# Optimization experiments

Hardware: AMD Instinct MI355X
Metric: run time of the kernel (lower is better)

## Reference

```python
import jax, jax.numpy as jnp
import numpy as np


def _att(xf, W1, W2):
    # xf: [B, L, dk]; low-rank attention scores, softmax over last dim
    dk = W1.shape[0]
    s1 = xf @ W1                                   # [B, L, 10]
    s2 = jnp.einsum('rk,bjk->brj', W2, xf)         # [B, 10, L]
    scores = jnp.einsum('bir,brj->bij', s1, s2) / jnp.sqrt(jnp.float32(dk))
    return jax.nn.softmax(scores, axis=-1)         # [B, L, L]


def setup_inputs() -> dict:
    B, Ci, Co, N, T = 8, 64, 64, 1000, 24
    ks = jax.random.split(jax.random.key(0), 16)
    f32 = jnp.float32
    return {
        'x': jax.random.normal(ks[0], (B, Ci, N, T), f32),
        'A_adj': jax.random.uniform(ks[1], (N, N), f32),
        'att0_W1': jax.random.normal(ks[2], (N * T, 10), f32) * 0.02,
        'att0_W2': jax.random.normal(ks[3], (10, N * T), f32) * 0.02,
        'gatt_W1': jax.random.normal(ks[4], (Ci * T, 10), f32) * 0.02,
        'gatt_W2': jax.random.normal(ks[5], (10, Ci * T), f32) * 0.02,
        'gcn_W': jax.random.normal(ks[6], (Ci, Co), f32) * 0.05,
        'tatt_W1': jax.random.normal(ks[7], (N * Co, 10), f32) * 0.02,
        'tatt_W2': jax.random.normal(ks[8], (10, N * Co), f32) * 0.02,
        'conv1_w': jax.random.normal(ks[9], (Co, Co, 1, 2), f32) * 0.05,
        'conv1_b': jax.random.normal(ks[10], (Co,), f32) * 0.05,
        'conv2_w': jax.random.normal(ks[11], (Co, Co, 1, 2), f32) * 0.05,
        'conv2_b': jax.random.normal(ks[12], (Co,), f32) * 0.05,
        'res_w': jax.random.normal(ks[13], (Co, Ci, 1, 1), f32) * 0.05,
        'res_b': jax.random.normal(ks[14], (Co,), f32) * 0.05,
        'ln_g': jnp.ones((Co,), f32),
        'ln_b': jnp.zeros((Co,), f32),
    }


def reference(x, A_adj, att0_W1, att0_W2, gatt_W1, gatt_W2, gcn_W,
              tatt_W1, tatt_W2, conv1_w, conv1_b, conv2_w, conv2_b,
              res_w, res_b, ln_g, ln_b):
    B, C, N, T = x.shape
    # ---- block-level channel attention (requires_value=True) ----
    xf = x.reshape(B, C, N * T)
    x1 = (_att(xf, att0_W1, att0_W2) @ xf).reshape(B, C, N, T)
    # ---- GCN block: attention-gated adjacency + graph matmul ----
    xg = jnp.transpose(x1, (0, 2, 1, 3)).reshape(B, N, C * T)
    Ag = _att(xg, gatt_W1, gatt_W2) * A_adj                  # [B, N, N]
    g1 = jnp.einsum('bnm,bcmt->bnct', Ag, x1)                # [B, N, C, T]
    g = jnp.einsum('bnct,co->bont', g1, gcn_W)               # [B, Co, N, T]
    Co = g.shape[1]
    # ---- TCN block: temporal attention + dilated causal convs ----
    xt = jnp.transpose(g, (0, 3, 2, 1)).reshape(B, T, N * Co)
    x2 = (_att(xt, tatt_W1, tatt_W2) @ xt).reshape(B, T, N, Co)
    x2 = jnp.transpose(x2, (0, 3, 2, 1))                     # [B, Co, N, T]
    for w, b, d in ((conv1_w, conv1_b, 1), (conv2_w, conv2_b, 2)):
        y = jax.lax.conv_general_dilated(
            x2, w, (1, 1), [(0, 0), (d, d)], rhs_dilation=(1, d),
            dimension_numbers=('NCHW', 'OIHW', 'NCHW'))
        y = y + b[None, :, None, None]
        x2 = jax.nn.relu(y[..., :-d])                        # trim to T
    # ---- 1x1 residual conv ----
    res = jnp.einsum('bcnt,oc->bont', x, res_w[:, :, 0, 0]) + res_b[None, :, None, None]
    out = jax.nn.relu(x2 + res)
    # ---- LayerNorm over channel dim ----
    o = jnp.transpose(out, (0, 3, 2, 1))                     # [B, T, N, Co]
    mu = o.mean(-1, keepdims=True)
    var = o.var(-1, keepdims=True)
    o = (o - mu) / jnp.sqrt(var + 1e-5) * ln_g + ln_b
    return jnp.transpose(o, (0, 3, 2, 1))                    # [B, Co, N, T]
```

## Files before the change

### kernel.cpp

```cpp
#include <hip/hip_runtime.h>
#include <hip/hip_bf16.h>

typedef unsigned int u32;
typedef unsigned short ushortt;

#define B_  8
#define C_  64
#define N_  1000
#define T_  24
#define R_  10
#define NT_ 24000
#define CT_ 1536
#define NC_ 64000

typedef __attribute__((ext_vector_type(8))) short bf8v;
typedef __attribute__((ext_vector_type(4))) float f4v;

__device__ __forceinline__ ushortt f2b_bits(float f) {
  u32 x = __float_as_uint(f);
  u32 r = (x + 0x7fffu + ((x >> 16) & 1u)) >> 16;
  return (ushortt)r;
}

__device__ __forceinline__ float blockSum256(float v, float* red) {
  red[threadIdx.x] = v; __syncthreads();
  #pragma unroll
  for (int s = 128; s > 0; s >>= 1) {
    if (threadIdx.x < s) red[threadIdx.x] += red[threadIdx.x + s];
    __syncthreads();
  }
  float r = red[0]; __syncthreads();
  return r;
}
__device__ __forceinline__ float blockMax256(float v, float* red) {
  red[threadIdx.x] = v; __syncthreads();
  #pragma unroll
  for (int s = 128; s > 0; s >>= 1) {
    if (threadIdx.x < s) red[threadIdx.x] = fmaxf(red[threadIdx.x], red[threadIdx.x + s]);
    __syncthreads();
  }
  float r = red[0]; __syncthreads();
  return r;
}

__device__ __forceinline__ void ld24f32(const float* p, float* v) {
  #pragma unroll
  for (int t = 0; t < 24; t += 4) {
    float4 f = *(const float4*)&p[t];
    v[t] = f.x; v[t+1] = f.y; v[t+2] = f.z; v[t+3] = f.w;
  }
}

__global__ __launch_bounds__(256) void zerok(float* p, int n) {
  int i = blockIdx.x * 256 + threadIdx.x;
  if (i < n) p[i] = 0.f;
}

__global__ __launch_bounds__(256) void pack_w(
    const float* __restrict__ W1, const float* __restrict__ W2,
    float* __restrict__ Wp, int K) {
  int i = blockIdx.x * 256 + threadIdx.x;
  if (i >= K * 20) return;
  int k = i / 20, r = i - k * 20;
  Wp[i] = (r < 10) ? W1[(size_t)k * 10 + r] : W2[(size_t)(r - 10) * K + k];
}

__global__ __launch_bounds__(256) void pack_tailw(
    const float* __restrict__ c1w, const float* __restrict__ c2w,
    const float* __restrict__ rw, ushortt* __restrict__ Wt) {
  int i = blockIdx.x * 256 + threadIdx.x;
  if (i >= 20480) return;
  float v;
  if (i < 8192) {
    int tap = i >> 12, o = (i >> 6) & 63, c = i & 63;
    v = c1w[(size_t)(o * 64 + c) * 2 + (tap ? 0 : 1)];
  } else if (i < 16384) {
    int j = i - 8192;
    int tap = j >> 12, o = (j >> 6) & 63, c = j & 63;
    v = c2w[(size_t)(o * 64 + c) * 2 + (tap ? 0 : 1)];
  } else {
    int j = i - 16384;
    v = rw[j];
  }
  Wt[i] = f2b_bits(v);
}

__global__ __launch_bounds__(256) void att0_s12(
    const float* __restrict__ x, const float* __restrict__ Wp,
    float* __restrict__ s1, float* __restrict__ s2) {
  __shared__ float red[40 * 257];
  const int row0 = blockIdx.x * 4;
  const int kbase = blockIdx.y * 6000;
  const int tid = threadIdx.x;
  float acc[4][20];
  #pragma unroll
  for (int r = 0; r < 4; ++r)
    #pragma unroll
    for (int j = 0; j < 20; ++j) acc[r][j] = 0.f;
  const float* xb = x + (size_t)row0 * NT_ + kbase;
  const float4* wb4 = (const float4*)Wp + (size_t)kbase * 5;
  #pragma unroll 1
  for (int it = 0; it < 6; ++it) {
    int slot = tid + 256 * it;
    if (slot < 1500) {
      int k = slot * 4;
      float4 xv0 = *(const float4*)&xb[k];
      float4 xv1 = *(const float4*)&xb[NT_ + k];
      float4 xv2 = *(const float4*)&xb[2 * NT_ + k];
      float4 xv3 = *(const float4*)&xb[3 * NT_ + k];
      const float4* w4 = wb4 + (size_t)slot * 20;
      #pragma unroll
      for (int kk = 0; kk < 4; ++kk) {
        float4 wa = w4[kk * 5 + 0], wbv = w4[kk * 5 + 1], wc = w4[kk * 5 + 2],
               wd = w4[kk * 5 + 3], we = w4[kk * 5 + 4];
        float w[20] = {wa.x,wa.y,wa.z,wa.w, wbv.x,wbv.y,wbv.z,wbv.w,
                       wc.x,wc.y,wc.z,wc.w, wd.x,wd.y,wd.z,wd.w,
                       we.x,we.y,we.z,we.w};
        float xs0 = ((const float*)&xv0)[kk];
        float xs1 = ((const float*)&xv1)[kk];
        float xs2 = ((const float*)&xv2)[kk];
        float xs3 = ((const float*)&xv3)[kk];
        #pragma unroll
        for (int j = 0; j < 20; ++j) {
          acc[0][j] += xs0 * w[j];
          acc[1][j] += xs1 * w[j];
          acc[2][j] += xs2 * w[j];
          acc[3][j] += xs3 * w[j];
        }
      }
    }
  }
  #pragma unroll
  for (int half = 0; half < 2; ++half) {
    __syncthreads();
    #pragma unroll
    for (int mm = 0; mm < 40; ++mm) {
      int m = half * 40 + mm;
      red[mm * 257 + tid] = acc[m / 20][m % 20];
    }
    __syncthreads();
    #pragma unroll
    for (int s = 128; s >= 8; s >>= 1) {
      for (int i = tid; i < 40 * s; i += 256) {
        int rr = i / s, col = i - rr * s;
        red[rr * 257 + col] += red[rr * 257 + col + s];
      }
      __syncthreads();
    }
    if (tid < 40) {
      float v = 0.f;
      #pragma unroll
      for (int c = 0; c < 8; ++c) v += red[tid * 257 + c];
      int m = half * 40 + tid;
      int row = row0 + m / 20, j = m % 20;
      if (j < 10) atomicAdd(&s1[row * 10 + j], v);
      else        atomicAdd(&s2[row * 10 + (j - 10)], v);
    }
  }
}

__global__ __launch_bounds__(64) void att0_softmax(
    const float* __restrict__ s1, const float* __restrict__ s2, float* __restrict__ P) {
  int b = blockIdx.x, i = threadIdx.x;
  float r1[R_];
  #pragma unroll
  for (int r = 0; r < R_; ++r) r1[r] = s1[(b * 64 + i) * R_ + r];
  const float scale = rsqrtf(24000.f);
  float row[64]; float m = -1e30f;
  for (int j = 0; j < 64; ++j) {
    const float* s2r = s2 + (size_t)(b * 64 + j) * R_;
    float d = 0.f;
    #pragma unroll
    for (int r = 0; r < R_; ++r) d += r1[r] * s2r[r];
    d *= scale; row[j] = d; m = fmaxf(m, d);
  }
  float s = 0.f;
  for (int j = 0; j < 64; ++j) { float e = __expf(row[j] - m); row[j] = e; s += e; }
  float inv = 1.f / s;
  for (int j = 0; j < 64; ++j) P[((size_t)b * 64 + i) * 64 + j] = row[j] * inv;
}

__global__ __launch_bounds__(256) void att0_apply(
    const float* __restrict__ x, const float* __restrict__ P, float* __restrict__ x1tr) {
  __shared__ float Pss[4160];
  __shared__ float xt[6144];
  int b = blockIdx.y, n0 = blockIdx.x * 4;
  int tid = threadIdx.x;
  for (int i = tid; i < 4096; i += 256)
    Pss[(i >> 6) * 65 + (i & 63)] = P[(size_t)b * 4096 + i];
  {
    const float4* src4 = (const float4*)x;
    float4* dst4 = (float4*)xt;
    for (int i = tid; i < 1536; i += 256) {
      int j = i / 24, q = i - j * 24;
      dst4[i] = src4[(size_t)(b * 64 + j) * 6000 + n0 * 6 + q];
    }
  }
  __syncthreads();
  int ig = tid >> 4, ln = (tid >> 2) & 3, ts = tid & 3;
  float acc[4][6];
  #pragma unroll
  for (int ii = 0; ii < 4; ++ii)
    #pragma unroll
    for (int m = 0; m < 6; ++m) acc[ii][m] = 0.f;
  const float* base = &xt[ln * 24 + ts * 6];
  #pragma unroll 4
  for (int j = 0; j < 64; ++j) {
    float vj[6];
    #pragma unroll
    for (int m = 0; m < 6; ++m) vj[m] = base[j * 96 + m];
    #pragma unroll
    for (int ii = 0; ii < 4; ++ii) {
      float p = Pss[(ig * 4 + ii) * 65 + j];
      #pragma unroll
      for (int m = 0; m < 6; ++m) acc[ii][m] += p * vj[m];
    }
  }
  float* drow = x1tr + ((size_t)b * N_ + n0 + ln) * CT_ + ts * 6;
  #pragma unroll
  for (int ii = 0; ii < 4; ++ii) {
    float* d = drow + (ig * 4 + ii) * 24;
    *(float2*)&d[0] = make_float2(acc[ii][0], acc[ii][1]);
    *(float2*)&d[2] = make_float2(acc[ii][2], acc[ii][3]);
    *(float2*)&d[4] = make_float2(acc[ii][4], acc[ii][5]);
  }
}

__global__ __launch_bounds__(256) void transpose_x1(
    const float* __restrict__ x1tr, ushortt* __restrict__ Xbt) {
  __shared__ float s[64][65];
  int b = blockIdx.z, n0 = blockIdx.y * 64, c0 = blockIdx.x * 64;
  int tid = threadIdx.x;
  int r = tid >> 2, cc = (tid & 3) * 16;
  if (n0 + r < N_) {
    const float* src = x1tr + ((size_t)b * N_ + n0 + r) * CT_ + c0 + cc;
    #pragma unroll
    for (int i = 0; i < 16; i += 4) {
      float4 v = *(const float4*)&src[i];
      s[r][cc + i] = v.x; s[r][cc + i + 1] = v.y;
      s[r][cc + i + 2] = v.z; s[r][cc + i + 3] = v.w;
    }
  } else {
    #pragma unroll
    for (int i = 0; i < 16; ++i) s[r][cc + i] = 0.f;
  }
  __syncthreads();
  ushortt* dst = Xbt + ((size_t)b * CT_ + c0 + r) * 1024 + n0 + cc;
  #pragma unroll
  for (int i = 0; i < 16; ++i) dst[i] = f2b_bits(s[cc + i][r]);
}

__global__ __launch_bounds__(256) void gatt_s12(
    const float* __restrict__ xg, const float* __restrict__ Wp,
    float* __restrict__ s1, float* __restrict__ s2T) {
  __shared__ float xs[6144];
  __shared__ float red[5120];
  int bn0 = blockIdx.x * 4;
  int tid = threadIdx.x;
  {
    const float4* src4 = (const float4*)(xg + (size_t)bn0 * CT_);
    float4* dst4 = (float4*)xs;
    for (int i = tid; i < 1536; i += 256) dst4[i] = src4[i];
  }
  __syncthreads();
  int rid = tid >> 6, ks = tid & 63;
  float a[20];
  #pragma unroll
  for (int r = 0; r < 20; ++r) a[r] = 0.f;
  for (int k = ks; k < CT_; k += 64) {
    float xv = xs[rid * CT_ + k];
    const float4* wp4 = (const float4*)&Wp[(size_t)k * 20];
    float4 wa = wp4[0], wb = wp4[1], wc = wp4[2], wd = wp4[3], we = wp4[4];
    float wv[20] = {wa.x,wa.y,wa.z,wa.w, wb.x,wb.y,wb.z,wb.w, wc.x,wc.y,wc.z,wc.w,
                    wd.x,wd.y,wd.z,wd.w, we.x,we.y,we.z,we.w};
    #pragma unroll
    for (int r = 0; r < 20; ++r) a[r] += xv * wv[r];
  }
  #pragma unroll
  for (int r = 0; r < 20; ++r) red[tid * 20 + r] = a[r];
  __syncthreads();
  if (tid < 80) {
    int rid2 = tid / 20, r = tid % 20;
    float s = 0.f;
    for (int l = 0; l < 64; ++l) s += red[(rid2 * 64 + l) * 20 + r];
    int row = bn0 + rid2;
    int b = row / N_, n = row - b * N_;
    if (r < 10) s1[row * 10 + r] = s;
    else        s2T[((size_t)b * 10 + (r - 10)) * N_ + n] = s;
  }
}

__global__ __launch_bounds__(256) void gatt_scores(
    const float* __restrict__ s1, const float* __restrict__ s2T,
    const float* __restrict__ Aadj, ushortt* __restrict__ Agb) {
  __shared__ float p[N_];
  __shared__ float r1[R_];
  __shared__ float red[256];
  int b = blockIdx.x / N_, n = blockIdx.x % N_;
  if (threadIdx.x < R_) r1[threadIdx.x] = s1[((size_t)b * N_ + n) * R_ + threadIdx.x];
  __syncthreads();
  const float scale = rsqrtf(1536.f);
  const float* s2b = s2T + (size_t)b * 10 * N_;
  float lmax = -1e30f;
  for (int m = threadIdx.x; m < N_; m += 256) {
    float d = 0.f;
    #pragma unroll
    for (int r = 0; r < R_; ++r) d += r1[r] * s2b[r * N_ + m];
    d *= scale; p[m] = d; lmax = fmaxf(lmax, d);
  }
  float gmax = blockMax256(lmax, red);
  float lsum = 0.f;
  for (int m = threadIdx.x; m < N_; m += 256) {
    float e = __expf(p[m] - gmax); p[m] = e; lsum += e;
  }
  float gsum = blockSum256(lsum, red);
  float inv = 1.f / gsum;
  ushortt* agr = Agb + ((size_t)b * 1024 + n) * 1024;
  const float* ar = Aadj + (size_t)n * N_;
  for (int m = threadIdx.x; m < 1024; m += 256) {
    float v = (m < N_) ? p[m] * inv * ar[m] : 0.f;
    agr[m] = f2b_bits(v);
  }
}

__global__ __launch_bounds__(256) void gemm_mfma(
    const ushortt* __restrict__ Agb, const ushortt* __restrict__ Xbt,
    float* __restrict__ g1) {
  __shared__ ushortt As[4096];
  __shared__ ushortt Bs[4096];
  const int b = blockIdx.z;
  const int n0 = blockIdx.x * 128;
  const int m0 = blockIdx.y * 128;
  const ushortt* Ab = Agb + (size_t)b * 1024 * 1024;
  const ushortt* Bb = Xbt + (size_t)b * 1536 * 1024;
  const int tid = threadIdx.x;
  const int wave = tid >> 6, lane = tid & 63;
  const int wr = (wave >> 1) * 64, wc = (wave & 1) * 64;
  const int lrow = lane >> 2;
  const int lcol = (lane & 3) * 8;
  const int q = lane >> 4, l15 = lane & 15;

  f4v acc[4][4];
  #pragma unroll
  for (int i = 0; i < 4; ++i)
    #pragma unroll
    for (int j = 0; j < 4; ++j) acc[i][j] = (f4v){0.f, 0.f, 0.f, 0.f};

  const ushortt* gA = Ab + (size_t)(m0 + wave * 16 + lrow) * 1024 + lcol;
  const ushortt* gB = Bb + (size_t)(n0 + wave * 16 + lrow) * 1024 + lcol;
  ushortt* lA = &As[wave * 16 * 32];
  ushortt* lB = &Bs[wave * 16 * 32];

  for (int k0 = 0; k0 < 1024; k0 += 32) {
    __syncthreads();
    __builtin_amdgcn_global_load_lds(
      (const __attribute__((address_space(1))) void*)(gA + k0),
      (__attribute__((address_space(3))) void*)lA, 16, 0, 0);
    __builtin_amdgcn_global_load_lds(
      (const __attribute__((address_space(1))) void*)(gA + (size_t)64 * 1024 + k0),
      (__attribute__((address_space(3))) void*)(lA + 64 * 32), 16, 0, 0);
    __builtin_amdgcn_global_load_lds(
      (const __attribute__((address_space(1))) void*)(gB + k0),
      (__attribute__((address_space(3))) void*)lB, 16, 0, 0);
    __builtin_amdgcn_global_load_lds(
      (const __attribute__((address_space(1))) void*)(gB + (size_t)64 * 1024 + k0),
      (__attribute__((address_space(3))) void*)(lB + 64 * 32), 16, 0, 0);
    __syncthreads();
    bf8v af[4], bfr[4];
    #pragma unroll
    for (int i = 0; i < 4; ++i)
      af[i] = *(const bf8v*)&As[(wr + i * 16 + l15) * 32 + q * 8];
    #pragma unroll
    for (int j = 0; j < 4; ++j)
      bfr[j] = *(const bf8v*)&Bs[(wc + j * 16 + l15) * 32 + q * 8];
    #pragma unroll
    for (int i = 0; i < 4; ++i)
      #pragma unroll
      for (int j = 0; j < 4; ++j)
        acc[i][j] = __builtin_amdgcn_mfma_f32_16x16x32_bf16(af[i], bfr[j], acc[i][j], 0, 0, 0);
  }
  #pragma unroll
  for (int i = 0; i < 4; ++i) {
    int rbase = m0 + wr + i * 16 + q * 4;
    #pragma unroll
    for (int r = 0; r < 4; ++r) {
      int gm = rbase + r;
      if (gm < N_) {
        float* dst = g1 + ((size_t)b * N_ + gm) * CT_ + n0 + wc + l15;
        #pragma unroll
        for (int j = 0; j < 4; ++j) dst[j * 16] = acc[i][j][r];
      }
    }
  }
}

__global__ __launch_bounds__(256) void gcn_out(
    const float* __restrict__ g1, const float* __restrict__ W, float* __restrict__ g) {
  __shared__ float gs[6160];
  __shared__ float Ws[4096];
  int b = blockIdx.y, n0 = blockIdx.x * 4;
  int tid = threadIdx.x;
  {
    const float4* src4 = (const float4*)g1;
    float4* dst4 = (float4*)gs;
    for (int i = tid; i < 1536; i += 256) {
      int ln = i / 384, q = i - ln * 384;
      dst4[ln * 385 + q] = src4[(size_t)(b * N_ + n0 + ln) * 384 + q];
    }
  }
  for (int i = tid; i < 4096; i += 256) Ws[i] = W[i];
  __syncthreads();
  int og = tid >> 4, ln = (tid >> 2) & 3, ts = tid & 3;
  float acc[4][6];
  #pragma unroll
  for (int oo = 0; oo < 4; ++oo)
    #pragma unroll
    for (int m = 0; m < 6; ++m) acc[oo][m] = 0.f;
  const float* base = &gs[ln * 1540 + ts * 6];
  #pragma unroll 4
  for (int c = 0; c < 64; ++c) {
    float v[6];
    #pragma unroll
    for (int m = 0; m < 6; ++m) v[m] = base[c * 24 + m];
    float4 w4 = *(const float4*)&Ws[c * 64 + og * 4];
    float wv[4] = {w4.x, w4.y, w4.z, w4.w};
    #pragma unroll
    for (int oo = 0; oo < 4; ++oo)
      #pragma unroll
      for (int m = 0; m < 6; ++m) acc[oo][m] += wv[oo] * v[m];
  }
  #pragma unroll
  for (int oo = 0; oo < 4; ++oo) {
    int o = og * 4 + oo;
    float* d = g + (((size_t)(b * C_ + o)) * N_ + n0 + ln) * T_ + ts * 6;
    *(float2*)&d[0] = make_float2(acc[oo][0], acc[oo][1]);
    *(float2*)&d[2] = make_float2(acc[oo][2], acc[oo][3]);
    *(float2*)&d[4] = make_float2(acc[oo][4], acc[oo][5]);
  }
}

__global__ __launch_bounds__(256) void tatt_s12(
    const float* __restrict__ g, const float* __restrict__ Wp,
    float* __restrict__ s1, float* __restrict__ s2) {
  __shared__ float glds[12288];
  int b = blockIdx.y, n0 = blockIdx.x * 8;
  int tid = threadIdx.x;
  {
    const float4* src4 = (const float4*)g;
    float4* dst4 = (float4*)glds;
    for (int i = tid; i < 3072; i += 256) {
      int o = i / 48, q = i - o * 48;
      dst4[i] = src4[(size_t)(b * 64 + o) * 6000 + n0 * 6 + q];
    }
  }
  __syncthreads();
  if (tid < 240) {
    int pg = tid / 24, t = tid - pg * 24;
    float a1 = 0.f, a2 = 0.f;
    for (int o = 0; o < 64; ++o) {
      const float* gro = &glds[o * 192 + t];
      const float* wp = &Wp[(size_t)(n0 * 64 + o) * 20 + pg];
      #pragma unroll
      for (int nl = 0; nl < 8; ++nl) {
        float v = gro[nl * 24];
        a1 += v * wp[(size_t)nl * 64 * 20];
        a2 += v * wp[(size_t)nl * 64 * 20 + 10];
      }
    }
    atomicAdd(&s1[(b * T_ + t) * R_ + pg], a1);
    atomicAdd(&s2[(b * T_ + t) * R_ + pg], a2);
  }
}

__global__ __launch_bounds__(64) void tatt_softmax(
    const float* __restrict__ s1, const float* __restrict__ s2, float* __restrict__ Pt) {
  int b = blockIdx.x, t = threadIdx.x;
  if (t >= T_) return;
  float r1[R_];
  #pragma unroll
  for (int r = 0; r < R_; ++r) r1[r] = s1[(b * T_ + t) * R_ + r];
  const float scale = rsqrtf(64000.f);
  float row[T_]; float m = -1e30f;
  for (int j = 0; j < T_; ++j) {
    const float* s2r = s2 + (b * T_ + j) * R_;
    float d = 0.f;
    #pragma unroll
    for (int r = 0; r < R_; ++r) d += r1[r] * s2r[r];
    d *= scale; row[j] = d; m = fmaxf(m, d);
  }
  float s = 0.f;
  for (int j = 0; j < T_; ++j) { float e = __expf(row[j] - m); row[j] = e; s += e; }
  float inv = 1.f / s;
  for (int j = 0; j < T_; ++j) Pt[(b * T_ + t) * T_ + j] = row[j] * inv;
}

__global__ __launch_bounds__(256) void tatt_apply(
    const float* __restrict__ g, const float* __restrict__ Pt, float* __restrict__ x2) {
  __shared__ float P[576];
  int b = blockIdx.y;
  for (int i = threadIdx.x; i < 576; i += 256) P[i] = Pt[b * 576 + i];
  __syncthreads();
  int row = blockIdx.x * 256 + threadIdx.x;
  const float* gp = g + ((size_t)b * 64000 + row) * T_;
  float gr[T_];
  ld24f32(gp, gr);
  float out[T_];
  #pragma unroll
  for (int t = 0; t < T_; ++t) {
    float a = 0.f;
    const float* Pr = &P[t * T_];
    #pragma unroll
    for (int j = 0; j < T_; ++j) a += Pr[j] * gr[j];
    out[t] = a;
  }
  float* xp = x2 + ((size_t)b * 64000 + row) * T_;
  #pragma unroll
  for (int t = 0; t < T_; t += 4)
    *(float4*)&xp[t] = make_float4(out[t], out[t+1], out[t+2], out[t+3]);
}

#define CSB 1024
__global__ __launch_bounds__(256, 3) void tail_k(
    const float* __restrict__ x2, const float* __restrict__ x,
    const ushortt* __restrict__ Wt,
    const float* __restrict__ c1b, const float* __restrict__ c2b,
    const float* __restrict__ rb,
    const float* __restrict__ lg, const float* __restrict__ lb,
    float* __restrict__ outp) {
  __shared__ ushortt X2c[8192];
  __shared__ ushortt Y1c[8192];
  __shared__ ushortt Xrc[8192];
  __shared__ float mu[96], rs[96];
  ushortt* preS = X2c;
  int b = blockIdx.y, n0 = blockIdx.x * 4;
  int tid = threadIdx.x;
  int wave = tid >> 6, lane = tid & 63;
  int q = lane >> 4, l15 = lane & 15;

  for (int i = tid; i < 6144; i += 256) {
    int c = i / 96, rem = i - c * 96;
    int nl = rem / 24, t = rem - nl * 24;
    int col = nl * 32 + 2 + t;
    size_t gidx = ((size_t)(b * 64 + c) * 1000 + n0 + nl) * 24 + t;
    int li = (c >> 3) * CSB + col * 8 + (c & 7);
    X2c[li] = f2b_bits(x2[gidx]);
    Xrc[li] = f2b_bits(x[gidx]);
  }
  {
    int blk = tid >> 5, gi = tid & 31;
    int nl = gi >> 3, gs = gi & 7;
    int s = (gs < 2) ? gs : (24 + gs);
    int col = nl * 32 + s;
    uint4 z = make_uint4(0, 0, 0, 0);
    *(uint4*)&X2c[blk * CSB + col * 8] = z;
    *(uint4*)&Xrc[blk * CSB + col * 8] = z;
  }
  __syncthreads();

  f4v acc1[2][4];
  #pragma unroll
  for (int ct = 0; ct < 2; ++ct)
    #pragma unroll
    for (int mt = 0; mt < 4; ++mt) acc1[ct][mt] = (f4v){0.f, 0.f, 0.f, 0.f};
  #pragma unroll
  for (int ki = 0; ki < 2; ++ki) {
    bf8v a0[4], a1[4];
    #pragma unroll
    for (int mt = 0; mt < 4; ++mt) {
      a0[mt] = *(const bf8v*)&Wt[(mt * 16 + l15) * 64 + ki * 32 + q * 8];
      a1[mt] = *(const bf8v*)&Wt[4096 + (mt * 16 + l15) * 64 + ki * 32 + q * 8];
    }
    #pragma unroll
    for (int ct = 0; ct < 2; ++ct) {
      int col = wave * 32 + ct * 16 + l15;
      int colp = (col == 0) ? 0 : col - 1;
      bf8v bc = *(const bf8v*)&X2c[(ki * 4 + q) * CSB + col * 8];
      bf8v bp = *(const bf8v*)&X2c[(ki * 4 + q) * CSB + colp * 8];
      #pragma unroll
      for (int mt = 0; mt < 4; ++mt) {
        acc1[ct][mt] = __builtin_amdgcn_mfma_f32_16x16x32_bf16(a0[mt], bc, acc1[ct][mt], 0, 0, 0);
        acc1[ct][mt] = __builtin_amdgcn_mfma_f32_16x16x32_bf16(a1[mt], bp, acc1[ct][mt], 0, 0, 0);
      }
    }
  }
  #pragma unroll
  for (int ct = 0; ct < 2; ++ct) {
    int s = ct * 16 + l15;
    int col = wave * 32 + s;
    bool v = (s >= 2 && s <= 25);
    #pragma unroll
    for (int mt = 0; mt < 4; ++mt) {
      int o0 = mt * 16 + q * 4;
      float4 bb = *(const float4*)&c1b[o0];
      float y0 = v ? fmaxf(acc1[ct][mt][0] + bb.x, 0.f) : 0.f;
      float y1 = v ? fmaxf(acc1[ct][mt][1] + bb.y, 0.f) : 0.f;
      float y2 = v ? fmaxf(acc1[ct][mt][2] + bb.z, 0.f) : 0.f;
      float y3 = v ? fmaxf(acc1[ct][mt][3] + bb.w, 0.f) : 0.f;
      u32 lo = (u32)f2b_bits(y0) | ((u32)f2b_bits(y1) << 16);
      u32 hi = (u32)f2b_bits(y2) | ((u32)f2b_bits(y3) << 16);
      *(uint2*)&Y1c[(o0 >> 3) * CSB + col * 8 + (o0 & 7)] = make_uint2(lo, hi);
    }
  }
  __syncthreads();

  f4v accA[2][4], accR[2][4];
  #pragma unroll
  for (int ct = 0; ct < 2; ++ct)
    #pragma unroll
    for (int mt = 0; mt < 4; ++mt) {
      accA[ct][mt] = (f4v){0.f, 0.f, 0.f, 0.f};
      accR[ct][mt] = (f4v){0.f, 0.f, 0.f, 0.f};
    }
  #pragma unroll
  for (int ki = 0; ki < 2; ++ki) {
    bf8v c0[4], c1t[4], rrf[4];
    #pragma unroll
    for (int mt = 0; mt < 4; ++mt) {
      c0[mt]  = *(const bf8v*)&Wt[8192 + (mt * 16 + l15) * 64 + ki * 32 + q * 8];
      c1t[mt] = *(const bf8v*)&Wt[12288 + (mt * 16 + l15) * 64 + ki * 32 + q * 8];
      rrf[mt] = *(const bf8v*)&Wt[16384 + (mt * 16 + l15) * 64 + ki * 32 + q * 8];
    }
    #pragma unroll
    for (int ct = 0; ct < 2; ++ct) {
      int col = wave * 32 + ct * 16 + l15;
      int colp2 = (col < 2) ? col : col - 2;
      bf8v bc = *(const bf8v*)&Y1c[(ki * 4 + q) * CSB + col * 8];
      bf8v bp = *(const bf8v*)&Y1c[(ki * 4 + q) * CSB + colp2 * 8];
      bf8v bx = *(const bf8v*)&Xrc[(ki * 4 + q) * CSB + col * 8];
      #pragma unroll
      for (int mt = 0; mt < 4; ++mt) {
        accA[ct][mt] = __builtin_amdgcn_mfma_f32_16x16x32_bf16(c0[mt], bc, accA[ct][mt], 0, 0, 0);
        accA[ct][mt] = __builtin_amdgcn_mfma_f32_16x16x32_bf16(c1t[mt], bp, accA[ct][mt], 0, 0, 0);
        accR[ct][mt] = __builtin_amdgcn_mfma_f32_16x16x32_bf16(rrf[mt], bx, accR[ct][mt], 0, 0, 0);
      }
    }
  }
  float pre[2][4][4];
  #pragma unroll
  for (int ct = 0; ct < 2; ++ct) {
    int s = ct * 16 + l15;
    bool v = (s >= 2 && s <= 25);
    int p = wave * 24 + s - 2;
    #pragma unroll
    for (int mt = 0; mt < 4; ++mt) {
      int o0 = mt * 16 + q * 4;
      float4 b2 = *(const float4*)&c2b[o0];
      float4 rbv = *(const float4*)&rb[o0];
      float bb2[4] = {b2.x, b2.y, b2.z, b2.w};
      float brv[4] = {rbv.x, rbv.y, rbv.z, rbv.w};
      #pragma unroll
      for (int r = 0; r < 4; ++r) {
        float a = fmaxf(accA[ct][mt][r] + bb2[r], 0.f) + accR[ct][mt][r] + brv[r];
        pre[ct][mt][r] = fmaxf(a, 0.f);
      }
      if (v) {
        u32 lo = (u32)f2b_bits(pre[ct][mt][0]) | ((u32)f2b_bits(pre[ct][mt][1]) << 16);
        u32 hi = (u32)f2b_bits(pre[ct][mt][2]) | ((u32)f2b_bits(pre[ct][mt][3]) << 16);
        *(uint2*)&preS[p * 68 + o0] = make_uint2(lo, hi);
      }
    }
  }
  __syncthreads();
  if (tid < 96) {
    const ushortt* pr = &preS[tid * 68];
    float sm = 0.f, qq = 0.f;
    #pragma unroll 8
    for (int c = 0; c < 64; c += 2) {
      u32 u = *(const u32*)&pr[c];
      float v0 = __uint_as_float(u << 16);
      float v1 = __uint_as_float(u & 0xffff0000u);
      sm += v0 + v1; qq += v0 * v0 + v1 * v1;
    }
    float m = sm * (1.f / 64.f);
    mu[tid] = m;
    rs[tid] = rsqrtf(qq * (1.f / 64.f) - m * m + 1e-5f);
  }
  __syncthreads();
  #pragma unroll
  for (int ct = 0; ct < 2; ++ct) {
    int s = ct * 16 + l15;
    bool v = (s >= 2 && s <= 25);
    if (!v) continue;
    int p = wave * 24 + s - 2;
    int t = s - 2;
    float m = mu[p], rr = rs[p];
    #pragma unroll
    for (int mt = 0; mt < 4; ++mt) {
      int o0 = mt * 16 + q * 4;
      float4 g4 = *(const float4*)&lg[o0];
      float4 b4 = *(const float4*)&lb[o0];
      float gg[4] = {g4.x, g4.y, g4.z, g4.w};
      float bb[4] = {b4.x, b4.y, b4.z, b4.w};
      #pragma unroll
      for (int r = 0; r < 4; ++r) {
        int o = o0 + r;
        float val = (pre[ct][mt][r] - m) * rr * gg[r] + bb[r];
        outp[((size_t)(b * 64 + o) * 1000 + n0 + wave) * 24 + t] = val;
      }
    }
  }
}

extern "C" void kernel_launch(void* const* d_in, const int* in_sizes, int n_in,
                              void* d_out, int out_size, void* d_ws, size_t ws_size,
                              hipStream_t stream) {
  const float* x     = (const float*)d_in[0];
  const float* Aadj  = (const float*)d_in[1];
  const float* a0W1  = (const float*)d_in[2];
  const float* a0W2  = (const float*)d_in[3];
  const float* gW1   = (const float*)d_in[4];
  const float* gW2   = (const float*)d_in[5];
  const float* gcnW  = (const float*)d_in[6];
  const float* tW1   = (const float*)d_in[7];
  const float* tW2   = (const float*)d_in[8];
  const float* c1w   = (const float*)d_in[9];
  const float* c1b   = (const float*)d_in[10];
  const float* c2w   = (const float*)d_in[11];
  const float* c2b   = (const float*)d_in[12];
  const float* rw    = (const float*)d_in[13];
  const float* rb    = (const float*)d_in[14];
  const float* lng   = (const float*)d_in[15];
  const float* lnb   = (const float*)d_in[16];
  float* out = (float*)d_out;

  float* ws = (float*)d_ws;
  float* R1   = ws;
  float* U    = R1 + 12288000;
  float* D    = U + 12288000;
  float* s1_0 = D + 12288000;
  float* s2_0 = s1_0 + 5120;
  float* P0   = s2_0 + 5120;
  float* s1g  = P0 + 32768;
  float* s2gT = s1g + 80000;
  float* s1t  = s2gT + 80000;
  float* s2t  = s1t + 1920;
  float* Ptb  = s2t + 1920;
  float* Wp0  = Ptb + 4608;
  float* Wgp  = Wp0 + 480000;
  float* Wtp  = Wgp + 30720;
  float* Wtl  = Wtp + 1280000;
  ushortt* Xbt = (ushortt*)U;
  ushortt* Agb = (ushortt*)(U + 6291456);
  ushortt* Wtail = (ushortt*)Wtl;
  float* g = U;
  if (ws_size < (size_t)38876416 * 4) return;

  pack_w<<<1875, 256, 0, stream>>>(a0W1, a0W2, Wp0, 24000);
  pack_w<<<120, 256, 0, stream>>>(gW1, gW2, Wgp, 1536);
  pack_w<<<5000, 256, 0, stream>>>(tW1, tW2, Wtp, 64000);
  pack_tailw<<<80, 256, 0, stream>>>(c1w, c2w, rw, Wtail);
  zerok<<<40, 256, 0, stream>>>(s1_0, 10240);
  att0_s12<<<dim3(128, 4), 256, 0, stream>>>(x, Wp0, s1_0, s2_0);
  att0_softmax<<<8, 64, 0, stream>>>(s1_0, s2_0, P0);
  att0_apply<<<dim3(250, 8), 256, 0, stream>>>(x, P0, R1);
  gatt_s12<<<2000, 256, 0, stream>>>(R1, Wgp, s1g, s2gT);
  transpose_x1<<<dim3(24, 16, 8), 256, 0, stream>>>(R1, Xbt);
  gatt_scores<<<8000, 256, 0, stream>>>(s1g, s2gT, Aadj, Agb);
  gemm_mfma<<<dim3(12, 8, 8), 256, 0, stream>>>(Agb, Xbt, D);
  gcn_out<<<dim3(250, 8), 256, 0, stream>>>(D, gcnW, g);
  zerok<<<15, 256, 0, stream>>>(s1t, 3840);
  tatt_s12<<<dim3(125, 8), 256, 0, stream>>>(g, Wtp, s1t, s2t);
  tatt_softmax<<<8, 32, 0, stream>>>(s1t, s2t, Ptb);
  tatt_apply<<<dim3(250, 8), 256, 0, stream>>>(g, Ptb, R1);
  tail_k<<<dim3(250, 8), 256, 0, stream>>>(R1, x, Wtail, c1b, c2b, rb,
                                           lng, lnb, out);
}
```

Baseline: 587.0 us.

## Restructure temporal-attention projection with register tiles and in-block tree reduction

Rewrites tatt_s12 so each thread owns one output channel and node slice and accumulates a 4-timestep by 20-projection register tile from vectorized float4 loads of g and the packed weights. Partial sums are reduced across the block through shared memory before a few atomics per block. The grid grows from 125x8 to 50x6x8 blocks. The aim is to cut redundant weight loads and the heavy global atomic traffic of the old kernel. In exchange it adds a multi-pass shared-memory reduction with many barriers and an 80-float accumulator per thread that raises register pressure.

```diff
diff --git a/kernel.cpp b/kernel.cpp
--- a/kernel.cpp
+++ b/kernel.cpp
@@ -442,33 +442,57 @@
 __global__ __launch_bounds__(256) void tatt_s12(
     const float* __restrict__ g, const float* __restrict__ Wp,
     float* __restrict__ s1, float* __restrict__ s2) {
-  __shared__ float glds[12288];
-  int b = blockIdx.y, n0 = blockIdx.x * 8;
-  int tid = threadIdx.x;
-  {
-    const float4* src4 = (const float4*)g;
-    float4* dst4 = (float4*)glds;
-    for (int i = tid; i < 3072; i += 256) {
-      int o = i / 48, q = i - o * 48;
-      dst4[i] = src4[(size_t)(b * 64 + o) * 6000 + n0 * 6 + q];
-    }
-  }
-  __syncthreads();
-  if (tid < 240) {
-    int pg = tid / 24, t = tid - pg * 24;
-    float a1 = 0.f, a2 = 0.f;
-    for (int o = 0; o < 64; ++o) {
-      const float* gro = &glds[o * 192 + t];
-      const float* wp = &Wp[(size_t)(n0 * 64 + o) * 20 + pg];
-      #pragma unroll
-      for (int nl = 0; nl < 8; ++nl) {
-        float v = gro[nl * 24];
-        a1 += v * wp[(size_t)nl * 64 * 20];
-        a2 += v * wp[(size_t)nl * 64 * 20 + 10];
-      }
-    }
-    atomicAdd(&s1[(b * T_ + t) * R_ + pg], a1);
-    atomicAdd(&s2[(b * T_ + t) * R_ + pg], a2);
+  __shared__ float red[40 * 257];
+  const int b = blockIdx.z, t0 = blockIdx.y * 4, n0 = blockIdx.x * 20;
+  const int tid = threadIdx.x;
+  const int o = tid & 63, nl = tid >> 6;
+  float acc[4][20];
+  #pragma unroll
+  for (int tt = 0; tt < 4; ++tt)
+    #pragma unroll
+    for (int j = 0; j < 20; ++j) acc[tt][j] = 0.f;
+  const float* gb = g + (size_t)(b * 64 + o) * NT_ + t0;
+  #pragma unroll 1
+  for (int it = 0; it < 5; ++it) {
+    int n = n0 + it * 4 + nl;
+    float4 gv = *(const float4*)&gb[n * 24];
+    const float4* w4 = (const float4*)&Wp[(size_t)(n * 64 + o) * 20];
+    float4 wa = w4[0], wbv = w4[1], wc = w4[2], wd = w4[3], we = w4[4];
+    float w[20] = {wa.x,wa.y,wa.z,wa.w, wbv.x,wbv.y,wbv.z,wbv.w,
+                   wc.x,wc.y,wc.z,wc.w, wd.x,wd.y,wd.z,wd.w,
+                   we.x,we.y,we.z,we.w};
+    float gs[4] = {gv.x, gv.y, gv.z, gv.w};
+    #pragma unroll
+    for (int tt = 0; tt < 4; ++tt)
+      #pragma unroll
+      for (int j = 0; j < 20; ++j) acc[tt][j] += gs[tt] * w[j];
+  }
+  #pragma unroll
+  for (int half = 0; half < 2; ++half) {
+    __syncthreads();
+    #pragma unroll
+    for (int mm = 0; mm < 40; ++mm) {
+      int m = half * 40 + mm;
+      red[mm * 257 + tid] = acc[m / 20][m % 20];
+    }
+    __syncthreads();
+    #pragma unroll
+    for (int s = 128; s >= 8; s >>= 1) {
+      for (int i = tid; i < 40 * s; i += 256) {
+        int rr = i / s, col = i - rr * s;
+        red[rr * 257 + col] += red[rr * 257 + col + s];
+      }
+      __syncthreads();
+    }
+    if (tid < 40) {
+      float v = 0.f;
+      #pragma unroll
+      for (int c = 0; c < 8; ++c) v += red[tid * 257 + c];
+      int m = half * 40 + tid;
+      int t = t0 + m / 20, j = m % 20;
+      if (j < 10) atomicAdd(&s1[(b * T_ + t) * R_ + j], v);
+      else        atomicAdd(&s2[(b * T_ + t) * R_ + (j - 10)], v);
+    }
   }
 }
 
@@ -759,7 +783,7 @@
   gemm_mfma<<<dim3(12, 8, 8), 256, 0, stream>>>(Agb, Xbt, D);
   gcn_out<<<dim3(250, 8), 256, 0, stream>>>(D, gcnW, g);
   zerok<<<15, 256, 0, stream>>>(s1t, 3840);
-  tatt_s12<<<dim3(125, 8), 256, 0, stream>>>(g, Wtp, s1t, s2t);
+  tatt_s12<<<dim3(50, 6, 8), 256, 0, stream>>>(g, Wtp, s1t, s2t);
   tatt_softmax<<<8, 32, 0, stream>>>(s1t, s2t, Ptb);
   tatt_apply<<<dim3(250, 8), 256, 0, stream>>>(g, Ptb, R1);
   tail_k<<<dim3(250, 8), 256, 0, stream>>>(R1, x, Wtail, c1b, c2b, rb,
```

New measurement: 569.6 us. -3.0%, faster.
